# Performance work log

Measured on AMD Instinct MI355X. Metric: run time of the kernel, lower is better.

Reference implementation:

```python
import jax, jax.numpy as jnp
import numpy as np

B, S, EMBED, HEADS = 2, 2048, 2048, 16
HEAD_DIM = EMBED // HEADS  # 128


def setup_inputs() -> dict:
    key = jax.random.key(0)
    k1, k2, k3 = jax.random.split(key, 3)
    x = jax.random.normal(k1, (B, S, EMBED), dtype=jnp.float32)
    # qkv_proj: Linear(EMBED -> 3*EMBED, bias=False); stored as [in, out]
    w_qkv = jax.random.normal(k2, (EMBED, 3 * EMBED), dtype=jnp.float32) / np.float32(np.sqrt(EMBED))
    # out_proj: Linear(EMBED -> EMBED, bias=False)
    w_out = jax.random.normal(k3, (EMBED, EMBED), dtype=jnp.float32) / np.float32(np.sqrt(EMBED))
    return {"x": x, "w_qkv": w_qkv, "w_out": w_out}


def reference(x, w_qkv, w_out):
    b, s, e = x.shape
    h, d = HEADS, e // HEADS
    qkv = x @ w_qkv                                  # [b, s, 3e]
    q, k, v = jnp.split(qkv, 3, axis=-1)             # each [b, s, e]
    q = q.reshape(b, s, h, d).transpose(0, 2, 1, 3)  # [b, h, s, d]
    k = k.reshape(b, s, h, d).transpose(0, 2, 1, 3)
    v = v.reshape(b, s, h, d).transpose(0, 2, 1, 3)
    scale = jnp.asarray(1.0 / np.sqrt(d), dtype=q.dtype)
    scores = jnp.einsum('bhqd,bhkd->bhqk', q, k) * scale  # [b, h, s, s]
    causal = jnp.tril(jnp.ones((s, s), dtype=bool))
    scores = jnp.where(causal, scores, -jnp.inf)
    attn = jax.nn.softmax(scores, axis=-1)
    ctx = jnp.einsum('bhqk,bhkd->bhqd', attn, v)     # [b, h, s, d]
    ctx = ctx.transpose(0, 2, 1, 3).reshape(b, s, e)
    return ctx @ w_out
```

## Files before the change

### kernel.cpp

```cpp
#include <hip/hip_runtime.h>
#include <cstdint>

#define S_LEN 2048
#define EMB   2048
#define NHEAD 16
#define HDIM  128
#define MROWS 4096
#define NQKV  6144

typedef __bf16 bf16x8 __attribute__((ext_vector_type(8)));
typedef __bf16 bf16x4 __attribute__((ext_vector_type(4)));
typedef float  f32x4  __attribute__((ext_vector_type(4)));

#define MFMA16(a, b, c) __builtin_amdgcn_mfma_f32_16x16x32_bf16((a), (b), (c), 0, 0, 0)

__device__ __forceinline__ unsigned short f2bf(float f) {
  unsigned u = __builtin_bit_cast(unsigned, f);
  u += 0x7fffu + ((u >> 16) & 1u);
  return (unsigned short)(u >> 16);
}
__device__ __forceinline__ float bf2f(unsigned short u) {
  unsigned v = ((unsigned)u) << 16;
  return __builtin_bit_cast(float, v);
}

__device__ __forceinline__ void gl_lds16(const unsigned short* g, unsigned short* l) {
  __builtin_amdgcn_global_load_lds(
      (const __attribute__((address_space(1))) void*)(uintptr_t)g,
      (__attribute__((address_space(3))) void*)(unsigned int)(uintptr_t)l,
      16, 0, 0);
}

#define FENCE() asm volatile("" ::: "memory")
#define BARRIER() do { FENCE(); __builtin_amdgcn_s_barrier(); FENCE(); } while (0)

__global__ void cast_bf16(const float* __restrict__ in, unsigned short* __restrict__ out, int n) {
  int i = (blockIdx.x * 256 + threadIdx.x) * 4;
  if (i >= n) return;
  float4 v = *(const float4*)(in + i);
  ushort4 o;
  o.x = f2bf(v.x); o.y = f2bf(v.y); o.z = f2bf(v.z); o.w = f2bf(v.w);
  *(ushort4*)(out + i) = o;
}

__global__ void transpose_cast(const float* __restrict__ in, unsigned short* __restrict__ out,
                               int R, int C) {
  __shared__ float tile[32][33];
  int bx = blockIdx.x << 5;
  int by = blockIdx.y << 5;
  int tx = threadIdx.x, ty = threadIdx.y;
  for (int j = 0; j < 32; j += 8)
    tile[ty + j][tx] = in[(size_t)(by + ty + j) * C + bx + tx];
  __syncthreads();
  for (int j = 0; j < 32; j += 8)
    out[(size_t)(bx + ty + j) * R + by + tx] = f2bf(tile[tx][ty + j]);
}

template<int NCOL>
__device__ __forceinline__ void gemm_pipe2(const unsigned short* __restrict__ Ap,
                                           const unsigned short* __restrict__ Bp,
                                           int m0, int n0, f32x4 (&acc)[8][NCOL]) {
  constexpr int BN = 128 * NCOL;
  constexpr int BISS = 2 * NCOL;
  constexpr int NT = 32;
  extern __shared__ unsigned short lds[];
  unsigned short* Abuf = lds;
  unsigned short* Bbuf = lds + 16384;

  const int tid = threadIdx.x, w = tid >> 6, lane = tid & 63;
  const int fr = lane & 15, g = lane >> 4;
  const int srow = tid >> 3, jp = tid & 7;

  auto issueA = [&](int buf, int kk, int idx) {
    const int row = (idx << 6) + srow;
    gl_lds16(Ap + (size_t)(m0 + row) * 2048 + kk + ((jp ^ (row & 7)) << 3),
             Abuf + (buf << 13) + (row << 6) + (jp << 3));
  };
  auto issueB = [&](int buf, int kk, int idx) {
    const int row = (idx << 6) + srow;
    gl_lds16(Bp + (size_t)(n0 + row) * 2048 + kk + ((jp ^ (row & 7)) << 3),
             Bbuf + buf * (BN * 64) + (row << 6) + (jp << 3));
  };

#pragma unroll
  for (int i = 0; i < BISS; ++i) issueB(0, 0, i);
  issueA(0, 0, 0); issueA(0, 0, 1);
  issueB(1, 64, 0); issueB(1, 64, 1);
  asm volatile("s_waitcnt vmcnt(2)" ::: "memory");
  __builtin_amdgcn_s_barrier();
  FENCE();

  bf16x8 bfr[NCOL][2];
  for (int t = 0; t < NT; ++t) {
    const int cb = t & 1, nb = cb ^ 1;
    const unsigned short* Ab = Abuf + (cb << 13);
    const unsigned short* Bb = Bbuf + cb * (BN * 64);
    const int kn = (t + 1) << 6;
    const bool s1 = (t + 1 < NT), s2 = (t + 2 < NT);

    bf16x8 af[2][2];
#pragma unroll
    for (int c = 0; c < NCOL; ++c)
#pragma unroll
      for (int ks = 0; ks < 2; ++ks)
        bfr[c][ks] = *(const bf16x8*)(Bb + ((w * 16 * NCOL + c * 16 + fr) << 6) +
                                      ((((ks << 2) + g) ^ (fr & 7)) << 3));
#pragma unroll
    for (int rr = 0; rr < 2; ++rr)
#pragma unroll
      for (int ks = 0; ks < 2; ++ks)
        af[rr][ks] = *(const bf16x8*)(Ab + (((rr * 16) + fr) << 6) +
                                      ((((ks << 2) + g) ^ (fr & 7)) << 3));
    if (s1) {
      issueB(nb, kn, 2); issueB(nb, kn, 3);
      if (NCOL == 3) issueB(nb, kn, 4);
    }
    BARRIER();
    __builtin_amdgcn_s_setprio(1);
#pragma unroll
    for (int ks = 0; ks < 2; ++ks)
#pragma unroll
      for (int rr = 0; rr < 2; ++rr)
#pragma unroll
        for (int c = 0; c < NCOL; ++c)
          acc[rr][c] = MFMA16(af[rr][ks], bfr[c][ks], acc[rr][c]);
    __builtin_amdgcn_s_setprio(0);

#pragma unroll
    for (int rr = 0; rr < 2; ++rr)
#pragma unroll
      for (int ks = 0; ks < 2; ++ks)
        af[rr][ks] = *(const bf16x8*)(Ab + (((32 + rr * 16) + fr) << 6) +
                                      ((((ks << 2) + g) ^ (fr & 7)) << 3));
    if (s1) {
      if (NCOL == 3) issueB(nb, kn, 5);
      issueA(nb, kn, 0); issueA(nb, kn, 1);
    }
    BARRIER();
    __builtin_amdgcn_s_setprio(1);
#pragma unroll
    for (int ks = 0; ks < 2; ++ks)
#pragma unroll
      for (int rr = 0; rr < 2; ++rr)
#pragma unroll
        for (int c = 0; c < NCOL; ++c)
          acc[2 + rr][c] = MFMA16(af[rr][ks], bfr[c][ks], acc[2 + rr][c]);
    __builtin_amdgcn_s_setprio(0);

#pragma unroll
    for (int rr = 0; rr < 2; ++rr)
#pragma unroll
      for (int ks = 0; ks < 2; ++ks)
        af[rr][ks] = *(const bf16x8*)(Ab + (((64 + rr * 16) + fr) << 6) +
                                      ((((ks << 2) + g) ^ (fr & 7)) << 3));
    BARRIER();
    __builtin_amdgcn_s_setprio(1);
#pragma unroll
    for (int ks = 0; ks < 2; ++ks)
#pragma unroll
      for (int rr = 0; rr < 2; ++rr)
#pragma unroll
        for (int c = 0; c < NCOL; ++c)
          acc[4 + rr][c] = MFMA16(af[rr][ks], bfr[c][ks], acc[4 + rr][c]);
    __builtin_amdgcn_s_setprio(0);

#pragma unroll
    for (int rr = 0; rr < 2; ++rr)
#pragma unroll
      for (int ks = 0; ks < 2; ++ks)
        af[rr][ks] = *(const bf16x8*)(Ab + (((96 + rr * 16) + fr) << 6) +
                                      ((((ks << 2) + g) ^ (fr & 7)) << 3));
    if (s2) {
      const int kn2 = (t + 2) << 6;
      issueB(cb, kn2, 0); issueB(cb, kn2, 1);
      asm volatile("s_waitcnt vmcnt(2)" ::: "memory");
    } else if (s1) {
      asm volatile("s_waitcnt vmcnt(0)" ::: "memory");
    }
    BARRIER();
    __builtin_amdgcn_s_setprio(1);
#pragma unroll
    for (int ks = 0; ks < 2; ++ks)
#pragma unroll
      for (int rr = 0; rr < 2; ++rr)
#pragma unroll
        for (int c = 0; c < NCOL; ++c)
          acc[6 + rr][c] = MFMA16(af[rr][ks], bfr[c][ks], acc[6 + rr][c]);
    __builtin_amdgcn_s_setprio(0);
  }
}

__global__ __launch_bounds__(512, 2) void gemm_qkv9(const unsigned short* __restrict__ A,
                                                    const unsigned short* __restrict__ Bt,
                                                    unsigned short* __restrict__ Qo,
                                                    unsigned short* __restrict__ Ko,
                                                    unsigned short* __restrict__ Vt) {
  const int bid = blockIdx.x;
  const int wg = (bid & 7) * 64 + (bid >> 3);
  const int mt = wg & 31, nt = wg >> 5;
  const int m0 = mt << 7, n0 = nt * 384;
  f32x4 acc[8][3] = {};
  gemm_pipe2<3>(A, Bt, m0, n0, acc);

  const int tid = threadIdx.x, w = tid >> 6, lane = tid & 63;
  const int fr = lane & 15, g = lane >> 4;
  const int rowb = m0 & (S_LEN - 1);
  const int bbase = (m0 >> 11) * NHEAD;
  for (int r = 0; r < 8; ++r) {
    const int sl = rowb + r * 16 + (g << 2);
    for (int c = 0; c < 3; ++c) {
      const int ncol = n0 + w * 48 + c * 16;
      const int which = ncol >> 11;
      const int h = (ncol >> 7) & 15;
      const int d = (ncol & 127) + fr;
      const int bh = bbase + h;
      if (which == 2) {
        ushort4 pk;
        pk.x = f2bf(acc[r][c][0]); pk.y = f2bf(acc[r][c][1]);
        pk.z = f2bf(acc[r][c][2]); pk.w = f2bf(acc[r][c][3]);
        *(ushort4*)(Vt + ((size_t)bh * HDIM + d) * S_LEN + sl) = pk;
      } else {
        unsigned short* dst = which ? Ko : Qo;
        for (int q4 = 0; q4 < 4; ++q4)
          dst[((size_t)bh * S_LEN + sl + q4) * HDIM + d] = f2bf(acc[r][c][q4]);
      }
    }
  }
}

__global__ __launch_bounds__(512, 2) void gemm_out9(const unsigned short* __restrict__ A,
                                                    const unsigned short* __restrict__ Bt,
                                                    float* __restrict__ C) {
  const int bid = blockIdx.x;
  const int wg = (bid & 7) * 32 + (bid >> 3);
  const int mt = wg & 31, nt = wg >> 5;
  const int m0 = mt << 7, n0 = nt << 8;
  f32x4 acc[8][2] = {};
  gemm_pipe2<2>(A, Bt, m0, n0, acc);

  const int tid = threadIdx.x, w = tid >> 6, lane = tid & 63;
  const int fr = lane & 15, g = lane >> 4;
  for (int r = 0; r < 8; ++r) {
    const int row = m0 + r * 16 + (g << 2);
    for (int c = 0; c < 2; ++c) {
      const int col = n0 + w * 32 + c * 16 + fr;
      for (int q4 = 0; q4 < 4; ++q4)
        C[(size_t)(row + q4) * EMB + col] = acc[r][c][q4];
    }
  }
}

__global__ __launch_bounds__(256, 3) void attn(const unsigned short* __restrict__ Qg,
                                               const unsigned short* __restrict__ Kg,
                                               const unsigned short* __restrict__ Vtg,
                                               unsigned short* __restrict__ ctx,
                                               unsigned short* __restrict__ Opart,
                                               float* __restrict__ Lp) {
  __shared__ __align__(16) unsigned short SA[16384];
  __shared__ __align__(16) unsigned short Ps[8192];
  unsigned short* Qs = SA;
  unsigned short* Ks = SA;
  unsigned short* Vs = SA + 8192;

  const int blk = blockIdx.x;
  const int bh = blk & 31;
  const int t = blk >> 5;
  int qt, kt0, nkt, part;
  if (t < 8)       { qt = t;     kt0 = 0;  nkt = 2 * t + 2;       part = -1; }
  else if (t < 16) { qt = t;     kt0 = 0;  nkt = 16;              part = (bh << 3) + (qt - 8); }
  else             { qt = t - 8; kt0 = 16; nkt = 2 * qt - 14;     part = 256 + (bh << 3) + (qt - 8); }

  const int tid = threadIdx.x, wave = tid >> 6, lane = tid & 63;
  const int fr = lane & 15, g = lane >> 4;

  const unsigned short* qsrc = Qg + ((size_t)bh * S_LEN + (qt << 7)) * HDIM;
  for (int i = 0; i < 8; ++i) {
    int s0 = (i * 256 + tid) << 3;
    int q = s0 >> 7, jp = (s0 >> 3) & 15;
    gl_lds16(qsrc + (q << 7) + ((jp ^ (q & 15)) << 3), Qs + s0);
  }
  __builtin_amdgcn_s_waitcnt(0);
  __syncthreads();

  bf16x8 qf[2][4];
  for (int nbq = 0; nbq < 2; ++nbq)
    for (int kd = 0; kd < 4; ++kd) {
      int q = (wave << 5) + (nbq << 4) + fr;
      qf[nbq][kd] = *(const bf16x8*)(Qs + (q << 7) + ((((kd << 2) + g) ^ fr) << 3));
    }
  __syncthreads();

  float lsum[2] = {0.f, 0.f};
  f32x4 oacc[2][8] = {};
  const float scale = 0.08838834764831845f;

  const unsigned short* kbase = Kg + (size_t)bh * S_LEN * HDIM;
  const unsigned short* vbase = Vtg + (size_t)bh * HDIM * S_LEN;

  for (int kti = 0; kti < nkt; ++kti) {
    const int kt = kt0 + kti;
    const unsigned short* ks = kbase + ((size_t)kt << 6) * HDIM;
    const unsigned short* vs = vbase + (kt << 6);
    for (int i = 0; i < 4; ++i) {
      int s0 = (i * 256 + tid) << 3;
      int key = s0 >> 7, jk = (s0 >> 3) & 15;
      gl_lds16(ks + (key << 7) + ((jk ^ (key & 15)) << 3), Ks + s0);
      int d = s0 >> 6, jv = (s0 >> 3) & 7;
      gl_lds16(vs + (size_t)d * S_LEN + ((jv ^ (d & 7)) << 3), Vs + s0);
    }
    __builtin_amdgcn_s_waitcnt(0);
    __syncthreads();

    f32x4 sacc[2][4] = {};
    for (int kd = 0; kd < 4; ++kd)
      for (int kb = 0; kb < 4; ++kb) {
        bf16x8 kf = *(const bf16x8*)(Ks + (((kb << 4) + fr) << 7) + ((((kd << 2) + g) ^ fr) << 3));
        sacc[0][kb] = MFMA16(kf, qf[0][kd], sacc[0][kb]);
        sacc[1][kb] = MFMA16(kf, qf[1][kd], sacc[1][kb]);
      }

    const bool diag = (kt >= 2 * qt);
    for (int nbq = 0; nbq < 2; ++nbq) {
      const int qg = (qt << 7) + (wave << 5) + (nbq << 4) + fr;
      float sum = 0.f;
      for (int kb = 0; kb < 4; ++kb) {
        float p[4];
        for (int r = 0; r < 4; ++r) {
          float v = sacc[nbq][kb][r] * scale;
          if (diag) {
            int keyg = (kt << 6) + (kb << 4) + (g << 2) + r;
            if (keyg > qg) v = -__builtin_inff();
          }
          p[r] = __expf(v);
          sum += p[r];
        }
        ushort4 pk;
        pk.x = f2bf(p[0]); pk.y = f2bf(p[1]);
        pk.z = f2bf(p[2]); pk.w = f2bf(p[3]);
        *(ushort4*)(Ps + (((wave << 3) + (nbq << 2) + kb) << 8) + (lane << 2)) = pk;
      }
      lsum[nbq] += sum;
    }

    __builtin_amdgcn_s_waitcnt(0);

    for (int kc = 0; kc < 2; ++kc) {
      const int kbr = (kc << 1) + (g >> 1);
      bf16x8 ap[2];
      for (int h2 = 0; h2 < 2; ++h2) {
        const unsigned short* pb =
            Ps + (((wave << 3) + (h2 << 2) + kbr) << 8) + ((g & 1) << 7) + (fr << 2);
        bf16x4 a0 = *(const bf16x4*)pb;
        bf16x4 a1 = *(const bf16x4*)(pb + 64);
        bf16x8 a;
        a[0] = a0[0]; a[1] = a0[1]; a[2] = a0[2]; a[3] = a0[3];
        a[4] = a1[0]; a[5] = a1[1]; a[6] = a1[2]; a[7] = a1[3];
        ap[h2] = a;
      }
      for (int nd = 0; nd < 8; ++nd) {
        bf16x8 bv = *(const bf16x8*)(Vs + (((nd << 4) + fr) << 6) + ((((kc << 2) + g) ^ (fr & 7)) << 3));
        oacc[0][nd] = MFMA16(ap[0], bv, oacc[0][nd]);
        oacc[1][nd] = MFMA16(ap[1], bv, oacc[1][nd]);
      }
    }
    __syncthreads();
  }

  for (int nbq = 0; nbq < 2; ++nbq) {
    lsum[nbq] += __shfl_xor(lsum[nbq], 16);
    lsum[nbq] += __shfl_xor(lsum[nbq], 32);
  }

  if (part < 0) {
    const int b = bh >> 4, h = bh & 15;
    for (int mq = 0; mq < 2; ++mq)
      for (int r = 0; r < 4; ++r) {
        float lv = __shfl(lsum[mq], (lane & 48) | ((g << 2) + r));
        const float il = 1.0f / lv;
        const int s = (qt << 7) + (wave << 5) + (mq << 4) + (g << 2) + r;
        unsigned short* dst = ctx + ((size_t)(b * S_LEN + s) * EMB) + (h << 7);
        for (int nd = 0; nd < 8; ++nd)
          dst[(nd << 4) + fr] = f2bf(oacc[mq][nd][r] * il);
      }
  } else {
    unsigned short* Ob = Opart + ((size_t)part << 14);
    for (int mq = 0; mq < 2; ++mq)
      for (int r = 0; r < 4; ++r) {
        const int ql = (wave << 5) + (mq << 4) + (g << 2) + r;
        unsigned short* dst = Ob + (ql << 7);
        for (int nd = 0; nd < 8; ++nd)
          dst[(nd << 4) + fr] = f2bf(oacc[mq][nd][r]);
      }
    if (g == 0)
      for (int nbq = 0; nbq < 2; ++nbq) {
        const int ql = (wave << 5) + (nbq << 4) + fr;
        Lp[(part << 7) + ql] = lsum[nbq];
      }
  }
}

__global__ void attn_combine(const unsigned short* __restrict__ Op,
                             const float* __restrict__ Lp,
                             unsigned short* __restrict__ ctx) {
  const int tid = threadIdx.x;
  const int rid = blockIdx.x * 16 + (tid >> 4);
  const int l16 = tid & 15;
  const int bh = rid >> 10;
  const int qtl = (rid >> 7) & 7;
  const int ql = rid & 127;
  const int p = (bh << 3) + qtl;
  const float lA = Lp[(p << 7) + ql];
  const float lB = Lp[((256 + p) << 7) + ql];
  const float il = 1.0f / (lA + lB);
  const int d0 = l16 << 3;
  const unsigned short* a = Op + ((size_t)p << 14) + (ql << 7) + d0;
  const unsigned short* b = Op + ((size_t)(256 + p) << 14) + (ql << 7) + d0;
  const int bb = bh >> 4, h = bh & 15;
  const int s = ((qtl + 8) << 7) + ql;
  unsigned short* dst = ctx + ((size_t)(bb * S_LEN + s) * EMB) + (h << 7) + d0;
  ushort4 va0 = *(const ushort4*)a, va1 = *(const ushort4*)(a + 4);
  ushort4 vb0 = *(const ushort4*)b, vb1 = *(const ushort4*)(b + 4);
  ushort4 o0, o1;
  o0.x = f2bf((bf2f(va0.x) + bf2f(vb0.x)) * il);
  o0.y = f2bf((bf2f(va0.y) + bf2f(vb0.y)) * il);
  o0.z = f2bf((bf2f(va0.z) + bf2f(vb0.z)) * il);
  o0.w = f2bf((bf2f(va0.w) + bf2f(vb0.w)) * il);
  o1.x = f2bf((bf2f(va1.x) + bf2f(vb1.x)) * il);
  o1.y = f2bf((bf2f(va1.y) + bf2f(vb1.y)) * il);
  o1.z = f2bf((bf2f(va1.z) + bf2f(vb1.z)) * il);
  o1.w = f2bf((bf2f(va1.w) + bf2f(vb1.w)) * il);
  *(ushort4*)dst = o0;
  *(ushort4*)(dst + 4) = o1;
}

extern "C" void kernel_launch(void* const* d_in, const int* in_sizes, int n_in,
                              void* d_out, int out_size, void* d_ws, size_t ws_size,
                              hipStream_t stream) {
  const float* x    = (const float*)d_in[0];
  const float* wqkv = (const float*)d_in[1];
  const float* wout = (const float*)d_in[2];
  float* out = (float*)d_out;

  unsigned short* ws = (unsigned short*)d_ws;
  const size_t NELEM = (size_t)MROWS * EMB;
  unsigned short* xb    = ws;
  unsigned short* wqkvT = xb + NELEM;
  unsigned short* woutT = wqkvT + (size_t)NQKV * EMB;
  unsigned short* Q     = woutT + (size_t)EMB * EMB;
  unsigned short* K     = Q + NELEM;
  unsigned short* Vt    = K + NELEM;
  unsigned short* ctx   = xb;
  unsigned short* Opart = wqkvT;
  float* Lp = (float*)(Opart + ((size_t)512 << 14));

  static bool attr_done = false;
  if (!attr_done) {
    (void)hipFuncSetAttribute((const void*)gemm_qkv9,
                              hipFuncAttributeMaxDynamicSharedMemorySize, 131072);
    (void)hipFuncSetAttribute((const void*)gemm_out9,
                              hipFuncAttributeMaxDynamicSharedMemorySize, 98304);
    attr_done = true;
  }

  cast_bf16<<<8192, 256, 0, stream>>>(x, xb, (int)NELEM);
  transpose_cast<<<dim3(NQKV / 32, EMB / 32), dim3(32, 8), 0, stream>>>(wqkv, wqkvT, EMB, NQKV);
  transpose_cast<<<dim3(EMB / 32, EMB / 32), dim3(32, 8), 0, stream>>>(wout, woutT, EMB, EMB);
  gemm_qkv9<<<512, 512, 131072, stream>>>(xb, wqkvT, Q, K, Vt);
  attn<<<768, 256, 0, stream>>>(Q, K, Vt, ctx, Opart, Lp);
  attn_combine<<<2048, 256, 0, stream>>>(Opart, Lp, ctx);
  gemm_out9<<<256, 512, 98304, stream>>>(ctx, woutT, out);
}
```

Baseline: 362.6 us.

## Retile GEMM core to 256-row tiles with 4x2 wave grid and split K phases

Replaces the GEMM mainloop with a new core that uses 256-row M tiles and a 4x2 wave layout, each wave owning 64 rows by 16*WCOL columns, so both A and B fragments get reused across several MFMAs. QKV tiles change from 128x384 to 256x192 and out-proj tiles from 128x256 to 256x128. The loop is reorganised into four phases per K step, each with explicit lgkmcnt waits and sched barriers, and the A and B prefetch schedule is changed. This aims to cut LDS reads per MFMA and improve overlap, at the cost of more barriers per iteration and a different LDS footprint.

```diff
diff --git a/kernel.cpp b/kernel.cpp
--- a/kernel.cpp
+++ b/kernel.cpp
@@ -33,6 +33,8 @@
 
 #define FENCE() asm volatile("" ::: "memory")
 #define BARRIER() do { FENCE(); __builtin_amdgcn_s_barrier(); FENCE(); } while (0)
+#define LGKM0() do { asm volatile("s_waitcnt lgkmcnt(0)" ::: "memory"); \
+                     __builtin_amdgcn_sched_barrier(0); } while (0)
 
 __global__ void cast_bf16(const float* __restrict__ in, unsigned short* __restrict__ out, int n) {
   int i = (blockIdx.x * 256 + threadIdx.x) * 4;
@@ -56,160 +58,128 @@
     out[(size_t)(bx + ty + j) * R + by + tx] = f2bf(tile[tx][ty + j]);
 }
 
-template<int NCOL>
-__device__ __forceinline__ void gemm_pipe2(const unsigned short* __restrict__ Ap,
-                                           const unsigned short* __restrict__ Bp,
-                                           int m0, int n0, f32x4 (&acc)[8][NCOL]) {
-  constexpr int BN = 128 * NCOL;
-  constexpr int BISS = 2 * NCOL;
-  constexpr int NT = 32;
+template<int WCOL>
+__device__ __forceinline__ void gemm_core(const unsigned short* __restrict__ Ap,
+                                          const unsigned short* __restrict__ Bp,
+                                          int m0, int n0, f32x4 (&acc)[4][WCOL]) {
+  constexpr int BN  = 32 * WCOL;
+  constexpr int NBI = BN / 64;
+  constexpr int HC  = WCOL / 2;
+  constexpr int NT  = 32;
   extern __shared__ unsigned short lds[];
   unsigned short* Abuf = lds;
-  unsigned short* Bbuf = lds + 16384;
+  unsigned short* Bbuf = lds + 32768;
 
   const int tid = threadIdx.x, w = tid >> 6, lane = tid & 63;
   const int fr = lane & 15, g = lane >> 4;
+  const int wm = (w & 3) << 6;
+  const int wn = (w >> 2) * 16 * WCOL;
   const int srow = tid >> 3, jp = tid & 7;
 
   auto issueA = [&](int buf, int kk, int idx) {
     const int row = (idx << 6) + srow;
     gl_lds16(Ap + (size_t)(m0 + row) * 2048 + kk + ((jp ^ (row & 7)) << 3),
-             Abuf + (buf << 13) + (row << 6) + (jp << 3));
+             Abuf + (buf << 14) + (row << 6) + (jp << 3));
   };
   auto issueB = [&](int buf, int kk, int idx) {
     const int row = (idx << 6) + srow;
     gl_lds16(Bp + (size_t)(n0 + row) * 2048 + kk + ((jp ^ (row & 7)) << 3),
              Bbuf + buf * (BN * 64) + (row << 6) + (jp << 3));
   };
-
-#pragma unroll
-  for (int i = 0; i < BISS; ++i) issueB(0, 0, i);
-  issueA(0, 0, 0); issueA(0, 0, 1);
-  issueB(1, 64, 0); issueB(1, 64, 1);
-  asm volatile("s_waitcnt vmcnt(2)" ::: "memory");
-  __builtin_amdgcn_s_barrier();
-  FENCE();
-
-  bf16x8 bfr[NCOL][2];
+  bf16x8 af[4], bf[HC];
+  auto readA = [&](const unsigned short* Ab, int ks) {
+#pragma unroll
+    for (int r = 0; r < 4; ++r)
+      af[r] = *(const bf16x8*)(Ab + ((wm + r * 16 + fr) << 6) +
+                               ((((ks << 2) + g) ^ (fr & 7)) << 3));
+  };
+  auto readB = [&](const unsigned short* Bb, int ks, int half) {
+#pragma unroll
+    for (int c = 0; c < HC; ++c)
+      bf[c] = *(const bf16x8*)(Bb + ((wn + (half * HC + c) * 16 + fr) << 6) +
+                               ((((ks << 2) + g) ^ (fr & 7)) << 3));
+  };
+  auto mm = [&](int chalf) {
+    __builtin_amdgcn_s_setprio(1);
+#pragma unroll
+    for (int r = 0; r < 4; ++r)
+#pragma unroll
+      for (int c = 0; c < HC; ++c)
+        acc[r][chalf * HC + c] = MFMA16(af[r], bf[c], acc[r][chalf * HC + c]);
+    __builtin_amdgcn_s_setprio(0);
+  };
+
+#pragma unroll
+  for (int i = 0; i < NBI; ++i) issueB(0, 0, i);
+#pragma unroll
+  for (int i = 0; i < 4; ++i) issueA(0, 0, i);
+#pragma unroll
+  for (int i = 0; i < 4; ++i) issueA(1, 64, i);
+  asm volatile("s_waitcnt vmcnt(4)" ::: "memory");
+  BARRIER();
+
+#pragma unroll 2
   for (int t = 0; t < NT; ++t) {
     const int cb = t & 1, nb = cb ^ 1;
-    const unsigned short* Ab = Abuf + (cb << 13);
+    const unsigned short* Ab = Abuf + (cb << 14);
     const unsigned short* Bb = Bbuf + cb * (BN * 64);
-    const int kn = (t + 1) << 6;
-    const bool s1 = (t + 1 < NT), s2 = (t + 2 < NT);
-
-    bf16x8 af[2][2];
-#pragma unroll
-    for (int c = 0; c < NCOL; ++c)
-#pragma unroll
-      for (int ks = 0; ks < 2; ++ks)
-        bfr[c][ks] = *(const bf16x8*)(Bb + ((w * 16 * NCOL + c * 16 + fr) << 6) +
-                                      ((((ks << 2) + g) ^ (fr & 7)) << 3));
-#pragma unroll
-    for (int rr = 0; rr < 2; ++rr)
-#pragma unroll
-      for (int ks = 0; ks < 2; ++ks)
-        af[rr][ks] = *(const bf16x8*)(Ab + (((rr * 16) + fr) << 6) +
-                                      ((((ks << 2) + g) ^ (fr & 7)) << 3));
-    if (s1) {
-      issueB(nb, kn, 2); issueB(nb, kn, 3);
-      if (NCOL == 3) issueB(nb, kn, 4);
-    }
+
+    readA(Ab, 0);
+    readB(Bb, 0, 0);
+    if (t + 1 < NT) {
+#pragma unroll
+      for (int i = 0; i < NBI; ++i) issueB(nb, (t + 1) << 6, i);
+    }
+    BARRIER(); LGKM0();
+    mm(0);
     BARRIER();
-    __builtin_amdgcn_s_setprio(1);
-#pragma unroll
-    for (int ks = 0; ks < 2; ++ks)
-#pragma unroll
-      for (int rr = 0; rr < 2; ++rr)
-#pragma unroll
-        for (int c = 0; c < NCOL; ++c)
-          acc[rr][c] = MFMA16(af[rr][ks], bfr[c][ks], acc[rr][c]);
-    __builtin_amdgcn_s_setprio(0);
-
-#pragma unroll
-    for (int rr = 0; rr < 2; ++rr)
-#pragma unroll
-      for (int ks = 0; ks < 2; ++ks)
-        af[rr][ks] = *(const bf16x8*)(Ab + (((32 + rr * 16) + fr) << 6) +
-                                      ((((ks << 2) + g) ^ (fr & 7)) << 3));
-    if (s1) {
-      if (NCOL == 3) issueB(nb, kn, 5);
-      issueA(nb, kn, 0); issueA(nb, kn, 1);
-    }
+
+    readB(Bb, 0, 1);
+    BARRIER(); LGKM0();
+    mm(1);
     BARRIER();
-    __builtin_amdgcn_s_setprio(1);
-#pragma unroll
-    for (int ks = 0; ks < 2; ++ks)
-#pragma unroll
-      for (int rr = 0; rr < 2; ++rr)
-#pragma unroll
-        for (int c = 0; c < NCOL; ++c)
-          acc[2 + rr][c] = MFMA16(af[rr][ks], bfr[c][ks], acc[2 + rr][c]);
-    __builtin_amdgcn_s_setprio(0);
-
-#pragma unroll
-    for (int rr = 0; rr < 2; ++rr)
-#pragma unroll
-      for (int ks = 0; ks < 2; ++ks)
-        af[rr][ks] = *(const bf16x8*)(Ab + (((64 + rr * 16) + fr) << 6) +
-                                      ((((ks << 2) + g) ^ (fr & 7)) << 3));
+
+    readA(Ab, 1);
+    readB(Bb, 1, 0);
+    BARRIER(); LGKM0();
+    mm(0);
     BARRIER();
-    __builtin_amdgcn_s_setprio(1);
-#pragma unroll
-    for (int ks = 0; ks < 2; ++ks)
-#pragma unroll
-      for (int rr = 0; rr < 2; ++rr)
-#pragma unroll
-        for (int c = 0; c < NCOL; ++c)
-          acc[4 + rr][c] = MFMA16(af[rr][ks], bfr[c][ks], acc[4 + rr][c]);
-    __builtin_amdgcn_s_setprio(0);
-
-#pragma unroll
-    for (int rr = 0; rr < 2; ++rr)
-#pragma unroll
-      for (int ks = 0; ks < 2; ++ks)
-        af[rr][ks] = *(const bf16x8*)(Ab + (((96 + rr * 16) + fr) << 6) +
-                                      ((((ks << 2) + g) ^ (fr & 7)) << 3));
-    if (s2) {
-      const int kn2 = (t + 2) << 6;
-      issueB(cb, kn2, 0); issueB(cb, kn2, 1);
-      asm volatile("s_waitcnt vmcnt(2)" ::: "memory");
-    } else if (s1) {
+
+    readB(Bb, 1, 1);
+    if (t + 2 < NT) {
+#pragma unroll
+      for (int i = 0; i < 4; ++i) issueA(cb, (t + 2) << 6, i);
+      asm volatile("s_waitcnt vmcnt(4)" ::: "memory");
+    } else if (t + 1 < NT) {
       asm volatile("s_waitcnt vmcnt(0)" ::: "memory");
     }
+    BARRIER(); LGKM0();
+    mm(1);
     BARRIER();
-    __builtin_amdgcn_s_setprio(1);
-#pragma unroll
-    for (int ks = 0; ks < 2; ++ks)
-#pragma unroll
-      for (int rr = 0; rr < 2; ++rr)
-#pragma unroll
-        for (int c = 0; c < NCOL; ++c)
-          acc[6 + rr][c] = MFMA16(af[rr][ks], bfr[c][ks], acc[6 + rr][c]);
-    __builtin_amdgcn_s_setprio(0);
-  }
-}
-
-__global__ __launch_bounds__(512, 2) void gemm_qkv9(const unsigned short* __restrict__ A,
+  }
+}
+
+__global__ __launch_bounds__(512, 2) void gemm_qkvX(const unsigned short* __restrict__ A,
                                                     const unsigned short* __restrict__ Bt,
                                                     unsigned short* __restrict__ Qo,
                                                     unsigned short* __restrict__ Ko,
                                                     unsigned short* __restrict__ Vt) {
   const int bid = blockIdx.x;
   const int wg = (bid & 7) * 64 + (bid >> 3);
-  const int mt = wg & 31, nt = wg >> 5;
-  const int m0 = mt << 7, n0 = nt * 384;
-  f32x4 acc[8][3] = {};
-  gemm_pipe2<3>(A, Bt, m0, n0, acc);
+  const int mt = wg & 15, nt = wg >> 4;
+  const int m0 = mt << 8, n0 = nt * 192;
+  f32x4 acc[4][6] = {};
+  gemm_core<6>(A, Bt, m0, n0, acc);
 
   const int tid = threadIdx.x, w = tid >> 6, lane = tid & 63;
   const int fr = lane & 15, g = lane >> 4;
+  const int wm = (w & 3) << 6, wn = (w >> 2) * 96;
   const int rowb = m0 & (S_LEN - 1);
   const int bbase = (m0 >> 11) * NHEAD;
-  for (int r = 0; r < 8; ++r) {
-    const int sl = rowb + r * 16 + (g << 2);
-    for (int c = 0; c < 3; ++c) {
-      const int ncol = n0 + w * 48 + c * 16;
+  for (int r = 0; r < 4; ++r) {
+    const int sl = rowb + wm + r * 16 + (g << 2);
+    for (int c = 0; c < 6; ++c) {
+      const int ncol = n0 + wn + c * 16;
       const int which = ncol >> 11;
       const int h = (ncol >> 7) & 15;
       const int d = (ncol & 127) + fr;
@@ -228,22 +198,23 @@
   }
 }
 
-__global__ __launch_bounds__(512, 2) void gemm_out9(const unsigned short* __restrict__ A,
+__global__ __launch_bounds__(512, 2) void gemm_outX(const unsigned short* __restrict__ A,
                                                     const unsigned short* __restrict__ Bt,
                                                     float* __restrict__ C) {
   const int bid = blockIdx.x;
   const int wg = (bid & 7) * 32 + (bid >> 3);
-  const int mt = wg & 31, nt = wg >> 5;
-  const int m0 = mt << 7, n0 = nt << 8;
-  f32x4 acc[8][2] = {};
-  gemm_pipe2<2>(A, Bt, m0, n0, acc);
+  const int mt = wg & 15, nt = wg >> 4;
+  const int m0 = mt << 8, n0 = nt << 7;
+  f32x4 acc[4][4] = {};
+  gemm_core<4>(A, Bt, m0, n0, acc);
 
   const int tid = threadIdx.x, w = tid >> 6, lane = tid & 63;
   const int fr = lane & 15, g = lane >> 4;
-  for (int r = 0; r < 8; ++r) {
-    const int row = m0 + r * 16 + (g << 2);
-    for (int c = 0; c < 2; ++c) {
-      const int col = n0 + w * 32 + c * 16 + fr;
+  const int wm = (w & 3) << 6, wn = (w >> 2) * 64;
+  for (int r = 0; r < 4; ++r) {
+    const int row = m0 + wm + r * 16 + (g << 2);
+    for (int c = 0; c < 4; ++c) {
+      const int col = n0 + wn + c * 16 + fr;
       for (int q4 = 0; q4 < 4; ++q4)
         C[(size_t)(row + q4) * EMB + col] = acc[r][c][q4];
     }
@@ -455,9 +426,9 @@
 
   static bool attr_done = false;
   if (!attr_done) {
-    (void)hipFuncSetAttribute((const void*)gemm_qkv9,
-                              hipFuncAttributeMaxDynamicSharedMemorySize, 131072);
-    (void)hipFuncSetAttribute((const void*)gemm_out9,
+    (void)hipFuncSetAttribute((const void*)gemm_qkvX,
+                              hipFuncAttributeMaxDynamicSharedMemorySize, 114688);
+    (void)hipFuncSetAttribute((const void*)gemm_outX,
                               hipFuncAttributeMaxDynamicSharedMemorySize, 98304);
     attr_done = true;
   }
@@ -465,8 +436,8 @@
   cast_bf16<<<8192, 256, 0, stream>>>(x, xb, (int)NELEM);
   transpose_cast<<<dim3(NQKV / 32, EMB / 32), dim3(32, 8), 0, stream>>>(wqkv, wqkvT, EMB, NQKV);
   transpose_cast<<<dim3(EMB / 32, EMB / 32), dim3(32, 8), 0, stream>>>(wout, woutT, EMB, EMB);
-  gemm_qkv9<<<512, 512, 131072, stream>>>(xb, wqkvT, Q, K, Vt);
+  gemm_qkvX<<<512, 512, 114688, stream>>>(xb, wqkvT, Q, K, Vt);
   attn<<<768, 256, 0, stream>>>(Q, K, Vt, ctx, Opart, Lp);
   attn_combine<<<2048, 256, 0, stream>>>(Opart, Lp, ctx);
-  gemm_out9<<<256, 512, 98304, stream>>>(ctx, woutT, out);
-}
+  gemm_outX<<<256, 512, 98304, stream>>>(ctx, woutT, out);
+}
```

New measurement: 372.9 us. 2.8% more time.
